# Kernel tuning notes

Measured on AMD Instinct MI355X. Metric: run time of the kernel, lower is better.

Reference implementation:

```python
import jax, jax.numpy as jnp
import numpy as np

B_PARAM = 1.0
BAND_WIDTH = 0.5
LOSS_WEIGHT = 1.0
EPS_REL = 1e-5
EPS_NORM = 1e-12


def setup_inputs() -> dict:
    key = jax.random.key(0)
    k1, k2 = jax.random.split(key)
    images = jax.random.normal(k1, (1, 256, 96, 96), dtype=jnp.float32)
    gt = jax.random.normal(k2, (1, 256, 96, 96), dtype=jnp.float32)
    return {"images": images, "gt": gt}


def _cosine_raw_distance(i_feat, t_feat):
    # _create_using_dot_p: center both by mean of t over (n, h, w), L2-normalize
    # along channels, then pairwise dot products -> cosine distance in [0, 1].
    mean_t = jnp.mean(t_feat, axis=(0, 2, 3), keepdims=True)
    i_c = i_feat - mean_t
    t_c = t_feat - mean_t
    i_n = i_c / jnp.maximum(jnp.sqrt(jnp.sum(i_c * i_c, axis=1, keepdims=True)), EPS_NORM)
    t_n = t_c / jnp.maximum(jnp.sqrt(jnp.sum(t_c * t_c, axis=1, keepdims=True)), EPS_NORM)
    n, c, h, w = i_n.shape
    t_v = t_n.reshape(n, c, h * w)
    # dot[n, h, w, s] = sum_c i_n[n,c,h,w] * t_v[n,c,s]   (the conv2d 1x1 kernel trick)
    dot = jnp.einsum('nchw,ncs->nhws', i_n, t_v)
    dist = jnp.clip((1.0 - dot) / 2.0, 0.0, None)
    return dist  # [n, h, w, h*w]


def _cx_loss(i_feat, t_feat):
    raw = _cosine_raw_distance(i_feat, t_feat)                      # [n,h,w,s]
    # relative distance (Eq. 2): divide each row by its min over target positions
    rel = raw / (jnp.min(raw, axis=-1, keepdims=True) + EPS_REL)
    w = jnp.exp((B_PARAM - rel) / BAND_WIDTH)
    cx = w / jnp.sum(w, axis=-1, keepdims=True)                     # row softmax-like
    max_gt_sim = jnp.max(cx, axis=(1, 2))                           # [n, s]
    cs = jnp.mean(max_gt_sim, axis=1)                               # [n]
    loss = jnp.mean(-jnp.log(cs))
    return loss * LOSS_WEIGHT


def reference(images, gt):
    # use_vgg=False, crop_quarter=False, h*w <= max_1d_size**2 -> direct CX loss.
    return _cx_loss(images, gt)
```

## Files before the change

### kernel.cpp

```cpp
#include <hip/hip_runtime.h>
#include <hip/hip_bf16.h>

#define S 9216
#define C 256
#define NCT 6
#define NG  (NCT*8)
#define SCH 1152

typedef __bf16 bf16x8 __attribute__((ext_vector_type(8)));
typedef float f32x4 __attribute__((ext_vector_type(4)));
typedef unsigned short us8 __attribute__((ext_vector_type(8)));
typedef unsigned short us4 __attribute__((ext_vector_type(4)));

#define GLOAD_LDS16(g, l) __builtin_amdgcn_global_load_lds( \
    (const __attribute__((address_space(1))) void*)(g),     \
    (__attribute__((address_space(3))) void*)(l), 16, 0, 0)

#define A2C 2.8853900817779268f

__device__ __forceinline__ float bf2f(unsigned short u) {
    return __uint_as_float(((unsigned)u) << 16);
}
__device__ __forceinline__ unsigned short f2bfbits(float x) {
    __hip_bfloat16 h = __float2bfloat16(x);
    return *reinterpret_cast<unsigned short*>(&h);
}

__global__ __launch_bounds__(256) void k_mean(const float* __restrict__ gt,
                                              float* __restrict__ meanT) {
    const int c = blockIdx.x;
    const float* p = gt + (size_t)c * S;
    float s = 0.f;
    for (int i = threadIdx.x; i < S; i += 256) s += p[i];
    for (int m = 1; m < 64; m <<= 1) s += __shfl_xor(s, m, 64);
    __shared__ float red[4];
    if ((threadIdx.x & 63) == 0) red[threadIdx.x >> 6] = s;
    __syncthreads();
    if (threadIdx.x == 0)
        meanT[c] = (red[0] + red[1] + red[2] + red[3]) * (1.0f / S);
}

__global__ __launch_bounds__(256) void k_ssq(const float* __restrict__ img,
                                             const float* __restrict__ gt,
                                             const float* __restrict__ meanT,
                                             float* __restrict__ ssqP,
                                             float* __restrict__ rowmin,
                                             float* __restrict__ rowsum,
                                             float* __restrict__ colmaxLog) {
    __shared__ float sm[32];
    const int part = blockIdx.x & 7;
    const int sb   = blockIdx.x >> 3;
    const int t    = threadIdx.x;
    if (t < 32) sm[t] = meanT[part * 32 + t];
    const int s = sb * 256 + t;
    if (part == 0) {
        rowmin[s]    = __uint_as_float(0x7f800000u);
        rowsum[s]    = 0.f;
        colmaxLog[s] = 0.f;
    }
    __syncthreads();
    float si = 0.f, st = 0.f;
    #pragma unroll 8
    for (int k = 0; k < 32; ++k) {
        const int c = part * 32 + k;
        const float m  = sm[k];
        const float di = img[(size_t)c * S + s] - m;
        const float dt = gt [(size_t)c * S + s] - m;
        si += di * di;
        st += dt * dt;
    }
    ssqP[(size_t)part * S + s]       = si;
    ssqP[(size_t)(part + 8) * S + s] = st;
}

__global__ __launch_bounds__(256) void k_write(const float* __restrict__ img,
                                               const float* __restrict__ gt,
                                               const float* __restrict__ meanT,
                                               const float* __restrict__ ssqP,
                                               __hip_bfloat16* __restrict__ A,
                                               __hip_bfloat16* __restrict__ B) {
    __shared__ float sm[32];
    const int part = blockIdx.x & 7;
    const int sb   = blockIdx.x >> 3;
    const int t    = threadIdx.x;
    if (t < 32) sm[t] = meanT[part * 32 + t];
    __syncthreads();
    const int s = sb * 256 + t;
    float si = 0.f, st = 0.f;
    #pragma unroll
    for (int p = 0; p < 8; ++p) {
        si += ssqP[(size_t)p * S + s];
        st += ssqP[(size_t)(p + 8) * S + s];
    }
    const float ri = 1.0f / fmaxf(sqrtf(si), 1e-12f);
    const float rt = 1.0f / fmaxf(sqrtf(st), 1e-12f);
    const int c0 = part * 32;
    #pragma unroll
    for (int cc = 0; cc < 4; ++cc) {
        us8 va, vb;
        #pragma unroll
        for (int e = 0; e < 8; ++e) {
            const int c = c0 + cc * 8 + e;
            const float m = sm[cc * 8 + e];
            va[e] = f2bfbits((img[(size_t)c * S + s] - m) * ri);
            vb[e] = f2bfbits((gt [(size_t)c * S + s] - m) * rt);
        }
        *reinterpret_cast<us8*>(A + (size_t)s * C + c0 + cc * 8) = va;
        *reinterpret_cast<us8*>(B + (size_t)s * C + c0 + cc * 8) = vb;
    }
}

__global__ __launch_bounds__(256, 2) void k_gemm_store(const __hip_bfloat16* __restrict__ A,
                                                       const __hip_bfloat16* __restrict__ B,
                                                       float* __restrict__ rowmin,
                                                       __hip_bfloat16* __restrict__ Q) {
    __shared__ alignas(16) __hip_bfloat16 As[64 * 256];
    __shared__ alignas(16) __hip_bfloat16 Bs[2 * 256 * 32];
    const int tid  = threadIdx.x;
    const int lane = tid & 63;
    const int wid  = tid >> 6;
    const int orig = blockIdx.x;
    const int xcd  = orig & 7;
    const int q    = orig >> 3;
    const int colGroup = q / 18;
    const int strip    = xcd * 18 + (q % 18);
    const int rowBase = strip * 64;
    const int cb0     = colGroup * 1536;

    const int frow = lane & 15;
    const int kgrp = lane >> 4;

    {
        const int arow_lo = lane >> 5;
        const int achunk  = lane & 31;
        #pragma unroll
        for (int j = 0; j < 8; ++j) {
            const int row = wid * 16 + j * 2 + arow_lo;
            const int cc  = achunk ^ (row & 7);
            GLOAD_LDS16(A + (size_t)(rowBase + row) * C + cc * 8,
                        &As[(wid * 16 + j * 2) * 256 + lane * 8]);
        }
    }
    const int bcol_lo = lane >> 2;
    const int bchunk  = (lane & 3) ^ ((lane >> 3) & 3);
    #pragma unroll
    for (int g = 0; g < 2; ++g) {
        const int cb = cb0 + (g >> 3) * 256;
        const int kt = g & 7;
        #pragma unroll
        for (int i = 0; i < 4; ++i) {
            const int col = wid * 16 + i * 64 + bcol_lo;
            GLOAD_LDS16(B + (size_t)(cb + col) * C + kt * 32 + bchunk * 8,
                        &Bs[(g & 1) * 8192 + wid * 512 + i * 2048 + lane * 8]);
        }
    }

    const int bswz = (kgrp ^ ((frow >> 1) & 3)) * 8;

    float vmin[4][4];
    #pragma unroll
    for (int m = 0; m < 4; ++m)
        #pragma unroll
        for (int qq = 0; qq < 4; ++qq) vmin[m][qq] = 1e30f;

    for (int t = 0; t < NCT; ++t) {
        f32x4 acc[4][4] = {};
        #pragma unroll
        for (int kt = 0; kt < 8; ++kt) {
            const int g = t * 8 + kt;
            if (kt < 2 && t > 0)      asm volatile("s_waitcnt vmcnt(20)" ::: "memory");
            else if (g < NG - 1)      asm volatile("s_waitcnt vmcnt(4)"  ::: "memory");
            else                      asm volatile("s_waitcnt vmcnt(0)"  ::: "memory");
            __builtin_amdgcn_s_barrier();

            bf16x8 af[4], bfr[4];
            #pragma unroll
            for (int m = 0; m < 4; ++m) {
                const int row = m * 16 + frow;
                const int p   = (kt * 4 + kgrp) ^ (frow & 7);
                af[m] = *reinterpret_cast<const bf16x8*>(&As[row * 256 + p * 8]);
            }
            const int bbase = (g & 1) * 8192;
            #pragma unroll
            for (int n = 0; n < 4; ++n) {
                const int col = wid * 64 + n * 16 + frow;
                bfr[n] = *reinterpret_cast<const bf16x8*>(&Bs[bbase + col * 32 + bswz]);
            }
            #pragma unroll
            for (int m = 0; m < 4; ++m)
                #pragma unroll
                for (int n = 0; n < 4; ++n)
                    acc[m][n] = __builtin_amdgcn_mfma_f32_16x16x32_bf16(af[m], bfr[n], acc[m][n], 0, 0, 0);

            __builtin_amdgcn_s_barrier();

            if (g + 2 < NG) {
                const int g2 = g + 2;
                const int cb = cb0 + (g2 >> 3) * 256;
                const int k2 = g2 & 7;
                #pragma unroll
                for (int i = 0; i < 4; ++i) {
                    const int col = wid * 16 + i * 64 + bcol_lo;
                    GLOAD_LDS16(B + (size_t)(cb + col) * C + k2 * 32 + bchunk * 8,
                                &Bs[(g2 & 1) * 8192 + wid * 512 + i * 2048 + lane * 8]);
                }
            }
        }

        const int colBase = cb0 + t * 256;
        #pragma unroll
        for (int n = 0; n < 4; ++n) {
            const int cg = colBase + wid * 64 + n * 16 + frow;
            #pragma unroll
            for (int m = 0; m < 4; ++m) {
                us4 pk;
                #pragma unroll
                for (int qq = 0; qq < 4; ++qq) {
                    const float raw = fmaxf(0.5f * (1.0f - acc[m][n][qq]), 0.0f);
                    vmin[m][qq] = fminf(vmin[m][qq], raw);
                    pk[qq] = f2bfbits(raw);
                }
                *reinterpret_cast<us4*>(Q + (size_t)cg * S + rowBase + m * 16 + kgrp * 4) = pk;
            }
        }
    }

    #pragma unroll
    for (int m = 0; m < 4; ++m)
        #pragma unroll
        for (int qq = 0; qq < 4; ++qq) {
            float v = vmin[m][qq];
            v = fminf(v, __shfl_xor(v, 1, 64));
            v = fminf(v, __shfl_xor(v, 2, 64));
            v = fminf(v, __shfl_xor(v, 4, 64));
            v = fminf(v, __shfl_xor(v, 8, 64));
            if (frow == 0)
                atomicMin((unsigned int*)&rowmin[rowBase + m * 16 + kgrp * 4 + qq],
                          __float_as_uint(v));
        }
}

__global__ __launch_bounds__(256) void k_rowsum(const __hip_bfloat16* __restrict__ Q,
                                                const float* __restrict__ rowmin,
                                                float* __restrict__ rowsum) {
    __shared__ float sBrN[64];
    __shared__ float srs[64];
    const int t  = threadIdx.x;
    const int r0 = (blockIdx.x >> 3) * 64;
    const int s0 = (blockIdx.x & 7) * SCH;
    if (t < 64) {
        sBrN[t] = -A2C / (rowmin[r0 + t] + 1e-5f);
        srs[t]  = 0.f;
    }
    __syncthreads();
    const int roct = (t & 7) * 8;
    const int ss   = t >> 3;
    float brn[8];
    #pragma unroll
    for (int j = 0; j < 8; ++j) brn[j] = sBrN[roct + j];
    const __hip_bfloat16* base = Q + r0 + roct;

    float sums[8] = {};
    #pragma unroll 4
    for (int i = 0; i < SCH / 32; ++i) {
        const int s = s0 + ss + i * 32;
        const us8 v = *reinterpret_cast<const us8*>(base + (size_t)s * S);
        #pragma unroll
        for (int j = 0; j < 8; ++j)
            sums[j] += exp2f(fmaf(brn[j], bf2f(v[j]), A2C));
    }
    #pragma unroll
    for (int j = 0; j < 8; ++j) {
        float x = sums[j];
        x += __shfl_xor(x, 8, 64);
        x += __shfl_xor(x, 16, 64);
        x += __shfl_xor(x, 32, 64);
        if ((t & 63) < 8) atomicAdd(&srs[roct + j], x);
    }
    __syncthreads();
    if (t < 64) atomicAdd(&rowsum[r0 + t], srs[t]);
}

__global__ __launch_bounds__(256) void k_colmax(const __hip_bfloat16* __restrict__ Q,
                                                const float* __restrict__ rowmin,
                                                const float* __restrict__ rowsum,
                                                float* __restrict__ colmaxLog) {
    __shared__ float sBrN[64];
    __shared__ float sCA[64];
    const int t  = threadIdx.x;
    const int r0 = (blockIdx.x >> 3) * 64;
    const int s0 = (blockIdx.x & 7) * SCH;
    if (t < 64) {
        sBrN[t] = -A2C / (rowmin[r0 + t] + 1e-5f);
        sCA[t]  = A2C + 64.0f - __log2f(rowsum[r0 + t]);
    }
    __syncthreads();
    const int roct = (t & 7) * 8;
    const int ss   = t >> 3;
    float brn[8], ca[8];
    #pragma unroll
    for (int j = 0; j < 8; ++j) { brn[j] = sBrN[roct + j]; ca[j] = sCA[roct + j]; }
    const __hip_bfloat16* base = Q + r0 + roct;

    #pragma unroll 4
    for (int i = 0; i < SCH / 32; ++i) {
        const int s = s0 + ss + i * 32;
        const us8 v = *reinterpret_cast<const us8*>(base + (size_t)s * S);
        float mx = -1e30f;
        #pragma unroll
        for (int j = 0; j < 8; ++j)
            mx = fmaxf(mx, fmaf(brn[j], bf2f(v[j]), ca[j]));
        mx = fmaxf(mx, __shfl_xor(mx, 1, 64));
        mx = fmaxf(mx, __shfl_xor(mx, 2, 64));
        mx = fmaxf(mx, __shfl_xor(mx, 4, 64));
        if ((t & 7) == 0)
            atomicMax((unsigned int*)&colmaxLog[s], __float_as_uint(fmaxf(mx, 0.0f)));
    }
}

__global__ __launch_bounds__(256) void k_final(const float* __restrict__ colmaxLog,
                                               float* __restrict__ out) {
    float s = 0.f;
    for (int i = threadIdx.x; i < S; i += 256) s += exp2f(colmaxLog[i]);
    for (int m = 1; m < 64; m <<= 1) s += __shfl_xor(s, m, 64);
    __shared__ float red[4];
    if ((threadIdx.x & 63) == 0) red[threadIdx.x >> 6] = s;
    __syncthreads();
    if (threadIdx.x == 0) {
        const float total = red[0] + red[1] + red[2] + red[3];
        out[0] = -logf(total * (5.421010862427522e-20f / (float)S));
    }
}

extern "C" void kernel_launch(void* const* d_in, const int* in_sizes, int n_in,
                              void* d_out, int out_size, void* d_ws, size_t ws_size,
                              hipStream_t stream) {
    const float* img = (const float*)d_in[0];
    const float* gt  = (const float*)d_in[1];

    float* ws        = (float*)d_ws;
    float* meanT     = ws;
    float* rowmin    = ws + 256;
    float* rowsum    = rowmin + S;
    float* colmaxLog = rowsum + S;
    __hip_bfloat16* A = (__hip_bfloat16*)(colmaxLog + S);
    __hip_bfloat16* B = A + (size_t)S * C;
    __hip_bfloat16* Q = B + (size_t)S * C;
    float* ssqP = (float*)Q;
    float* out = (float*)d_out;

    k_mean <<<C, 256, 0, stream>>>(gt, meanT);
    k_ssq  <<<288, 256, 0, stream>>>(img, gt, meanT, ssqP, rowmin, rowsum, colmaxLog);
    k_write<<<288, 256, 0, stream>>>(img, gt, meanT, ssqP, A, B);

    k_gemm_store<<<864, 256, 0, stream>>>(A, B, rowmin, Q);
    k_rowsum<<<1152, 256, 0, stream>>>(Q, rowmin, rowsum);
    k_colmax<<<1152, 256, 0, stream>>>(Q, rowmin, rowsum, colmaxLog);

    k_final<<<1, 256, 0, stream>>>(colmaxLog, out);
}
```

Measured before the change: 218.9 us.

## Use per-wave triple-buffered B tiles to drop block barriers in GEMM loop

```diff
diff --git a/kernel.cpp b/kernel.cpp
--- a/kernel.cpp
+++ b/kernel.cpp
@@ -115,7 +115,7 @@
                                                        float* __restrict__ rowmin,
                                                        __hip_bfloat16* __restrict__ Q) {
     __shared__ alignas(16) __hip_bfloat16 As[64 * 256];
-    __shared__ alignas(16) __hip_bfloat16 Bs[2 * 256 * 32];
+    __shared__ alignas(16) __hip_bfloat16 Bs[4 * 3 * 2048];
     const int tid  = threadIdx.x;
     const int lane = tid & 63;
     const int wid  = tid >> 6;
@@ -141,19 +141,26 @@
                         &As[(wid * 16 + j * 2) * 256 + lane * 8]);
         }
     }
-    const int bcol_lo = lane >> 2;
-    const int bchunk  = (lane & 3) ^ ((lane >> 3) & 3);
-    #pragma unroll
-    for (int g = 0; g < 2; ++g) {
-        const int cb = cb0 + (g >> 3) * 256;
-        const int kt = g & 7;
-        #pragma unroll
-        for (int i = 0; i < 4; ++i) {
-            const int col = wid * 16 + i * 64 + bcol_lo;
-            GLOAD_LDS16(B + (size_t)(cb + col) * C + kt * 32 + bchunk * 8,
-                        &Bs[(g & 1) * 8192 + wid * 512 + i * 2048 + lane * 8]);
-        }
-    }
+
+    const int bcol4  = lane >> 2;
+    const int bchunk = (lane & 3) ^ ((lane >> 3) & 3);
+    __hip_bfloat16* const BsW = &Bs[wid * 6144];
+    const __hip_bfloat16* const Bsrc = B + (size_t)(cb0 + wid * 64) * C;
+
+#define STAGE_B(tt, kk, bb) do {                                              \
+    _Pragma("unroll")                                                         \
+    for (int i_ = 0; i_ < 4; ++i_) {                                          \
+        GLOAD_LDS16(Bsrc + (size_t)((tt) * 256 + i_ * 16 + bcol4) * C         \
+                         + (kk) * 32 + bchunk * 8,                            \
+                    &BsW[(bb) * 2048 + i_ * 512]);                            \
+    } } while (0)
+
+    STAGE_B(0, 0, 0);
+    STAGE_B(0, 1, 1);
+    STAGE_B(0, 2, 2);
+
+    asm volatile("s_waitcnt vmcnt(12)" ::: "memory");
+    __builtin_amdgcn_s_barrier();
 
     const int bswz = (kgrp ^ ((frow >> 1) & 3)) * 8;
 
@@ -163,15 +170,26 @@
         #pragma unroll
         for (int qq = 0; qq < 4; ++qq) vmin[m][qq] = 1e30f;
 
+    int b0 = 0;
     for (int t = 0; t < NCT; ++t) {
         f32x4 acc[4][4] = {};
         #pragma unroll
         for (int kt = 0; kt < 8; ++kt) {
-            const int g = t * 8 + kt;
-            if (kt < 2 && t > 0)      asm volatile("s_waitcnt vmcnt(20)" ::: "memory");
-            else if (g < NG - 1)      asm volatile("s_waitcnt vmcnt(4)"  ::: "memory");
-            else                      asm volatile("s_waitcnt vmcnt(0)"  ::: "memory");
-            __builtin_amdgcn_s_barrier();
+            if (kt < 3) {
+                if (t) asm volatile("s_waitcnt vmcnt(24)" ::: "memory");
+                else   asm volatile("s_waitcnt vmcnt(8)"  ::: "memory");
+            } else if (kt < 6) {
+                asm volatile("s_waitcnt vmcnt(8)" ::: "memory");
+            } else if (kt == 6) {
+                if (t == NCT - 1) asm volatile("s_waitcnt vmcnt(4)" ::: "memory");
+                else              asm volatile("s_waitcnt vmcnt(8)" ::: "memory");
+            } else {
+                if (t == NCT - 1) asm volatile("s_waitcnt vmcnt(0)" ::: "memory");
+                else              asm volatile("s_waitcnt vmcnt(8)" ::: "memory");
+            }
+
+            int bufc = b0 + (kt % 3);
+            if (bufc >= 3) bufc -= 3;
 
             bf16x8 af[4], bfr[4];
             #pragma unroll
@@ -180,32 +198,27 @@
                 const int p   = (kt * 4 + kgrp) ^ (frow & 7);
                 af[m] = *reinterpret_cast<const bf16x8*>(&As[row * 256 + p * 8]);
             }
-            const int bbase = (g & 1) * 8192;
             #pragma unroll
-            for (int n = 0; n < 4; ++n) {
-                const int col = wid * 64 + n * 16 + frow;
-                bfr[n] = *reinterpret_cast<const bf16x8*>(&Bs[bbase + col * 32 + bswz]);
+            for (int n = 0; n < 4; ++n)
+                bfr[n] = *reinterpret_cast<const bf16x8*>(
+                    &BsW[bufc * 2048 + (n * 16 + frow) * 32 + bswz]);
+
+            asm volatile("s_waitcnt lgkmcnt(0)" ::: "memory");
+            __builtin_amdgcn_sched_barrier(0);
+
+            if (kt <= 4) {
+                STAGE_B(t, kt + 3, bufc);
+            } else if (t + 1 < NCT) {
+                STAGE_B(t + 1, kt - 5, bufc);
             }
+
             #pragma unroll
             for (int m = 0; m < 4; ++m)
                 #pragma unroll
                 for (int n = 0; n < 4; ++n)
                     acc[m][n] = __builtin_amdgcn_mfma_f32_16x16x32_bf16(af[m], bfr[n], acc[m][n], 0, 0, 0);
-
-            __builtin_amdgcn_s_barrier();
-
-            if (g + 2 < NG) {
-                const int g2 = g + 2;
-                const int cb = cb0 + (g2 >> 3) * 256;
-                const int k2 = g2 & 7;
-                #pragma unroll
-                for (int i = 0; i < 4; ++i) {
-                    const int col = wid * 16 + i * 64 + bcol_lo;
-                    GLOAD_LDS16(B + (size_t)(cb + col) * C + k2 * 32 + bchunk * 8,
-                                &Bs[(g2 & 1) * 8192 + wid * 512 + i * 2048 + lane * 8]);
-                }
-            }
-        }
+        }
+        b0 += 2; if (b0 >= 3) b0 -= 3;
 
         const int colBase = cb0 + t * 256;
         #pragma unroll
@@ -224,6 +237,7 @@
             }
         }
     }
+#undef STAGE_B
 
     #pragma unroll
     for (int m = 0; m < 4; ++m)
```

Result: no change. 214.7 us (-1.9%).
